# Optimization experiments

Measured on AMD Instinct MI355X. Metric: run time of the kernel, lower is better.

Reference implementation:

```python
import jax, jax.numpy as jnp
import numpy as np

NUM_HEADS = 8
N_POINTS = 9
OFFSET_SCALE = 4.0


def bilinear_sample(fmap_flat, xy, H, W):
    """fmap_flat: (BH, H*W, C) row-major spatial; xy: (BH, S, 2) pixel coords (x, y).
    grid_sample(mode='bilinear', padding_mode='zeros', align_corners=True) equivalent.
    Returns (BH, S, C)."""
    x, y = xy[..., 0], xy[..., 1]
    x0 = jnp.floor(x); y0 = jnp.floor(y)
    x1 = x0 + 1.0;    y1 = y0 + 1.0
    wx1 = x - x0; wx0 = 1.0 - wx1
    wy1 = y - y0; wy0 = 1.0 - wy1

    def corner(xi, yi, wgt):
        valid = (xi >= 0) & (xi <= W - 1) & (yi >= 0) & (yi <= H - 1)
        xi_c = jnp.clip(xi, 0, W - 1).astype(jnp.int32)
        yi_c = jnp.clip(yi, 0, H - 1).astype(jnp.int32)
        idx = yi_c * W + xi_c                                   # (BH, S)
        vals = jnp.take_along_axis(fmap_flat, idx[..., None], axis=1)  # (BH, S, C)
        return vals * (wgt * valid.astype(fmap_flat.dtype))[..., None]

    return (corner(x0, y0, wx0 * wy0) + corner(x1, y0, wx1 * wy0)
            + corner(x0, y1, wx0 * wy1) + corner(x1, y1, wx1 * wy1))


def setup_inputs() -> dict:
    key = jax.random.key(0)
    ks = jax.random.split(key, 10)
    B, N, D = 4, 6400, 256
    Hh, P = NUM_HEADS, N_POINTS
    s = 0.02
    return {
        "x":    jax.random.normal(ks[0], (B, N, D), dtype=jnp.float32),
        "Wq":   jax.random.normal(ks[1], (D, D), dtype=jnp.float32) * s,
        "bq":   jnp.zeros((D,), jnp.float32),
        "Woff": jax.random.normal(ks[2], (Hh * P * 2, D), dtype=jnp.float32) * s,
        "boff": jax.random.normal(ks[3], (Hh * P * 2,), dtype=jnp.float32) * s,
        "Wkv":  jax.random.normal(ks[4], (2 * D, D), dtype=jnp.float32) * s,
        "bkv":  jnp.zeros((2 * D,), jnp.float32),
        "Wout": jax.random.normal(ks[5], (D, D), dtype=jnp.float32) * s,
        "bout": jnp.zeros((D,), jnp.float32),
        "h": 40,
        "w": 160,
    }


def reference(x, Wq, bq, Woff, boff, Wkv, bkv, Wout, bout, h, w):
    B, N, D = x.shape
    H, P = NUM_HEADS, N_POINTS
    hd = D // H

    # queries: (B, H, N, hd)
    q = (x @ Wq.T + bq).reshape(B, N, H, hd).transpose(0, 2, 1, 3)

    # per-query per-head offsets in pixels: (B, N, H, P, 2) (dx, dy)
    offsets = jnp.tanh(x @ Woff.T + boff).reshape(B, N, H, P, 2) * OFFSET_SCALE

    # K/V feature maps via 1x1 conv == per-token linear; split heads, flat spatial
    kv = x @ Wkv.T + bkv                     # (B, N, 2D)
    k = kv[..., :D]
    v = kv[..., D:]
    k_flat = k.reshape(B, N, H, hd).transpose(0, 2, 1, 3).reshape(B * H, N, hd)
    v_flat = v.reshape(B, N, H, hd).transpose(0, 2, 1, 3).reshape(B * H, N, hd)

    # base pixel grid (x, y), row-major over (h, w)
    ys, xs = jnp.meshgrid(jnp.arange(h, dtype=x.dtype), jnp.arange(w, dtype=x.dtype), indexing="ij")
    base_xy = jnp.stack([xs, ys], axis=-1).reshape(N, 2)

    # sampling locations: (B, N, H, P, 2) -> (B*H, N*P, 2)
    sample_xy = base_xy[None, :, None, None, :] + offsets
    sample_xy = sample_xy.transpose(0, 2, 1, 3, 4).reshape(B * H, N * P, 2)

    sampled_k = bilinear_sample(k_flat, sample_xy, h, w).reshape(B, H, N, P, hd)
    sampled_v = bilinear_sample(v_flat, sample_xy, h, w).reshape(B, H, N, P, hd)

    logits = jnp.einsum("bhnd,bhnpd->bhnp", q, sampled_k) * (hd ** -0.5)
    attn = jax.nn.softmax(logits, axis=-1)
    out = jnp.einsum("bhnp,bhnpd->bhnd", attn, sampled_v)   # (B, H, N, hd)
    out = out.transpose(0, 2, 1, 3).reshape(B, N, D)
    return out @ Wout.T + bout
```

## Files before the change

### kernel.cpp

```cpp
#include <hip/hip_runtime.h>
#include <math.h>

#define BSZ    4
#define NTOK   6400
#define DMODEL 256
#define NHEAD  8
#define HDIM   32
#define NPTS   9
#define HSP    40
#define WSP    160
#define KDIM   256
#define MTOT   (BSZ*NTOK)

typedef short  short8  __attribute__((ext_vector_type(8)));
typedef float  floatx4 __attribute__((ext_vector_type(4)));
typedef float  f32x2   __attribute__((ext_vector_type(2)));

__device__ __forceinline__ ushort f2bf(float f) {
    uint u = __float_as_uint(f);
    u = (u + 0x7FFFu + ((u >> 16) & 1u)) >> 16;
    return (ushort)u;
}

__device__ __forceinline__ void unpack8v(uint4 u, f32x2* f) {
    f[0].x = __uint_as_float(u.x << 16); f[0].y = __uint_as_float(u.x & 0xFFFF0000u);
    f[1].x = __uint_as_float(u.y << 16); f[1].y = __uint_as_float(u.y & 0xFFFF0000u);
    f[2].x = __uint_as_float(u.z << 16); f[2].y = __uint_as_float(u.z & 0xFFFF0000u);
    f[3].x = __uint_as_float(u.w << 16); f[3].y = __uint_as_float(u.w & 0xFFFF0000u);
}

__device__ __forceinline__ float dot8(uint4 u, const f32x2* q2) {
    f32x2 a; a.x = 0.f; a.y = 0.f;
    f32x2 t;
    t.x = __uint_as_float(u.x << 16); t.y = __uint_as_float(u.x & 0xFFFF0000u);
    a += t * q2[0];
    t.x = __uint_as_float(u.y << 16); t.y = __uint_as_float(u.y & 0xFFFF0000u);
    a += t * q2[1];
    t.x = __uint_as_float(u.z << 16); t.y = __uint_as_float(u.z & 0xFFFF0000u);
    a += t * q2[2];
    t.x = __uint_as_float(u.w << 16); t.y = __uint_as_float(u.w & 0xFFFF0000u);
    a += t * q2[3];
    return a.x + a.y;
}

#define AS1C(p) ((const __attribute__((address_space(1))) void*)(p))
#define AS3(p)  ((__attribute__((address_space(3))) void*)(p))

__global__ __launch_bounds__(256) void cast_all(
    const float* __restrict__ x,   const float* __restrict__ Wq,
    const float* __restrict__ Woff,const float* __restrict__ Wkv,
    const float* __restrict__ Wout,
    ushort* __restrict__ xb, ushort* __restrict__ wf, ushort* __restrict__ woutb)
{
    const int bid = blockIdx.x;
    const int o = (bid < 1600) ? ((bid >> 3) + (bid & 7) * 200) : bid;
    if (o >= 1625 && o < 1632) {
        const int i = (o - 1625) * 4096 + threadIdx.x * 4;
        ushort4 z; z.x = 0; z.y = 0; z.z = 0; z.w = 0;
        #pragma unroll
        for (int k = 0; k < 4; ++k)
            *(ushort4*)(wf + 400 * 256 + i + k * 1024) = z;
        return;
    }
    const float* src; ushort* dst; int base;
    if      (o < 1600) { src = x;    dst = xb;              base = o; }
    else if (o < 1616) { src = Wq;   dst = wf;              base = o - 1600; }
    else if (o < 1625) { src = Woff; dst = wf + 256 * 256;  base = o - 1616; }
    else if (o < 1664) { src = Wkv;  dst = wf + 512 * 256;  base = o - 1632; }
    else               { src = Wout; dst = woutb;           base = o - 1664; }
    const int i0 = base * 4096 + threadIdx.x * 4;
    float4 v[4];
    #pragma unroll
    for (int k = 0; k < 4; ++k) v[k] = *(const float4*)(src + i0 + k * 1024);
    #pragma unroll
    for (int k = 0; k < 4; ++k) {
        ushort4 o4;
        o4.x = f2bf(v[k].x); o4.y = f2bf(v[k].y);
        o4.z = f2bf(v[k].z); o4.w = f2bf(v[k].w);
        *(ushort4*)(dst + i0 + k * 1024) = o4;
    }
}

template <int MODE>
__global__ __launch_bounds__(256) void gemm64(
    const ushort* __restrict__ Xb,
    const ushort* __restrict__ Wf,
    const float* __restrict__ bq, const float* __restrict__ boff,
    const float* __restrict__ bkv,
    ushort* __restrict__ qb, float* __restrict__ off,
    ushort* __restrict__ kfb, ushort* __restrict__ vfb,
    float* __restrict__ Yout)
{
    constexpr int NBN = (MODE == 0) ? 16 : 4;
    __shared__ ushort As[2][64 * 64];
    __shared__ ushort Bs[2][64 * 64];

    const int tid = threadIdx.x;
    const int bid = blockIdx.x;
    const int xcd = bid & 7;
    const int j   = bid >> 3;
    const int block_n = (j % NBN) * 64;
    const int block_m = (xcd * 50 + j / NBN) * 64;

    const int wave = tid >> 6, lane = tid & 63;
    const int wr = (wave >> 1) * 32, wc = (wave & 1) * 32;
    const int l15 = lane & 15, quad = lane >> 4;

    const int srow  = lane >> 3;
    const int sslot = (lane & 7) ^ srow;

    floatx4 acc[2][2];
    #pragma unroll
    for (int i = 0; i < 2; ++i)
        #pragma unroll
        for (int jj = 0; jj < 2; ++jj) {
            acc[i][jj][0] = 0.f; acc[i][jj][1] = 0.f;
            acc[i][jj][2] = 0.f; acc[i][jj][3] = 0.f;
        }

    auto stage = [&](int buf, int kt) {
        #pragma unroll
        for (int i = 0; i < 2; ++i) {
            const int rb = wave * 16 + i * 8;
            const ushort* sa = Xb + (size_t)(block_m + rb + srow) * KDIM + kt + sslot * 8;
            const ushort* sb = Wf + (size_t)(block_n + rb + srow) * KDIM + kt + sslot * 8;
            __builtin_amdgcn_global_load_lds(AS1C(sa), AS3(&As[buf][rb * 64]), 16, 0, 0);
            __builtin_amdgcn_global_load_lds(AS1C(sb), AS3(&Bs[buf][rb * 64]), 16, 0, 0);
        }
    };

    auto compute = [&](int buf) {
        #pragma unroll
        for (int ks2 = 0; ks2 < 2; ++ks2) {
            short8 af[2], bfr[2];
            #pragma unroll
            for (int f = 0; f < 2; ++f) {
                const int ra  = wr + f * 16 + l15;
                const int rbb = wc + f * 16 + l15;
                const int sl  = (((ks2 * 4 + quad) ^ (l15 & 7))) * 8;
                af[f]  = *(const short8*)&As[buf][ra * 64 + sl];
                bfr[f] = *(const short8*)&Bs[buf][rbb * 64 + sl];
            }
            #pragma unroll
            for (int fm = 0; fm < 2; ++fm)
                #pragma unroll
                for (int fn = 0; fn < 2; ++fn)
                    acc[fm][fn] = __builtin_amdgcn_mfma_f32_16x16x32_bf16(
                        af[fm], bfr[fn], acc[fm][fn], 0, 0, 0);
        }
    };

    stage(0, 0);
    __syncthreads();
    #pragma unroll
    for (int t = 0; t < 3; ++t) {
        stage((t + 1) & 1, (t + 1) * 64);
        compute(t & 1);
        __syncthreads();
    }
    compute(1);

    const int bb  = block_m / NTOK;
    const int nn0 = block_m - bb * NTOK;
    #pragma unroll
    for (int fn = 0; fn < 2; ++fn) {
        const int col = block_n + wc + fn * 16 + l15;
        float bcol;
        if (MODE == 1) {
            bcol = bq[col];
        } else {
            if      (col < 256) bcol = bq[col];
            else if (col < 400) bcol = boff[col - 256];
            else if (col < 512) bcol = 0.f;
            else                bcol = bkv[col - 512];
        }
        #pragma unroll
        for (int fm = 0; fm < 2; ++fm) {
            #pragma unroll
            for (int r = 0; r < 4; ++r) {
                const int rloc = wr + fm * 16 + quad * 4 + r;
                const int row  = block_m + rloc;
                const float val = acc[fm][fn][r] + bcol;
                if (MODE == 1) {
                    Yout[(size_t)row * DMODEL + col] = val;
                } else {
                    if (col < 256) {
                        qb[(size_t)row * DMODEL + col] = f2bf(val);
                    } else if (col < 400) {
                        off[(size_t)row * 144 + (col - 256)] = tanhf(val) * 4.0f;
                    } else if (col >= 512) {
                        const int c2 = col - 512;
                        const int hh = (c2 & 255) >> 5, cc = c2 & 31;
                        const int nn = nn0 + rloc;
                        const size_t o = (((size_t)(bb * NHEAD + hh)) * NTOK + nn) * HDIM + cc;
                        if (c2 < 256) kfb[o] = f2bf(val);
                        else          vfb[o] = f2bf(val);
                    }
                }
            }
        }
    }
}

__global__ __launch_bounds__(256, 3) void deform_attn(
    const ushort* __restrict__ qb,
    const float* __restrict__ off,
    const ushort* __restrict__ kfb,
    const ushort* __restrict__ vfb,
    ushort* __restrict__ attnb)
{
    const int lane = threadIdx.x & 63;
    const int o = ((int)blockIdx.x >> 3) + ((int)blockIdx.x & 7) * 400;
    const int token = o * 8 + (threadIdx.x >> 6) * 2 + (lane >> 5);
    const int h = (lane >> 2) & 7, lc = lane & 3;
    const int b = token / NTOK, n = token % NTOK;

    const uint4 qu = *(const uint4*)(qb + (size_t)token * DMODEL + h * HDIM + lc * 8);
    f32x2 q2[4]; unpack8v(qu, q2);

    const float* ob = off + (size_t)token * 144 + h * (NPTS * 2);
    const float bx = (float)(n % WSP), by = (float)(n / WSP);
    const ushort* kbase = kfb + (size_t)(b * NHEAD + h) * NTOK * HDIM + lc * 8;
    const ushort* vbase = vfb + (size_t)(b * NHEAD + h) * NTOK * HDIM + lc * 8;

    float s = 0.f;
    f32x2 o2[4];
    #pragma unroll
    for (int i = 0; i < 4; ++i) { o2[i].x = 0.f; o2[i].y = 0.f; }

    #pragma unroll
    for (int g = 0; g < 3; ++g) {
        int   idx[3][4];
        float wt[3][4];
        #pragma unroll
        for (int jj = 0; jj < 3; ++jj) {
            const int p = g * 3 + jj;
            const float2 of = *(const float2*)(ob + 2 * p);
            const float sx = bx + of.x, sy = by + of.y;
            const float fx0 = floorf(sx), fy0 = floorf(sy);
            const float wx1 = sx - fx0, wx0 = 1.0f - wx1;
            const float wy1 = sy - fy0, wy0 = 1.0f - wy1;
            const int ix0 = (int)fx0, iy0 = (int)fy0;
            const int ix1 = ix0 + 1, iy1 = iy0 + 1;
            const bool vx0 = (ix0 >= 0) & (ix0 <= WSP - 1);
            const bool vx1 = (ix1 >= 0) & (ix1 <= WSP - 1);
            const bool vy0 = (iy0 >= 0) & (iy0 <= HSP - 1);
            const bool vy1 = (iy1 >= 0) & (iy1 <= HSP - 1);
            const int cx0 = min(max(ix0, 0), WSP - 1);
            const int cx1 = min(max(ix1, 0), WSP - 1);
            const int cy0 = min(max(iy0, 0), HSP - 1);
            const int cy1 = min(max(iy1, 0), HSP - 1);
            wt[jj][0] = wx0 * wy0 * (float)(vx0 && vy0);
            wt[jj][1] = wx1 * wy0 * (float)(vx1 && vy0);
            wt[jj][2] = wx0 * wy1 * (float)(vx0 && vy1);
            wt[jj][3] = wx1 * wy1 * (float)(vx1 && vy1);
            idx[jj][0] = (cy0 * WSP + cx0) * HDIM;
            idx[jj][1] = (cy0 * WSP + cx1) * HDIM;
            idx[jj][2] = (cy1 * WSP + cx0) * HDIM;
            idx[jj][3] = (cy1 * WSP + cx1) * HDIM;
        }

        uint4 ku[12], vu[12];
        #pragma unroll
        for (int jj = 0; jj < 3; ++jj)
            #pragma unroll
            for (int c = 0; c < 4; ++c)
                ku[jj * 4 + c] = *(const uint4*)(kbase + idx[jj][c]);
        #pragma unroll
        for (int jj = 0; jj < 3; ++jj)
            #pragma unroll
            for (int c = 0; c < 4; ++c)
                vu[jj * 4 + c] = *(const uint4*)(vbase + idx[jj][c]);

        float l[3];
        #pragma unroll
        for (int jj = 0; jj < 3; ++jj) {
            float part = wt[jj][0] * dot8(ku[jj * 4 + 0], q2)
                       + wt[jj][1] * dot8(ku[jj * 4 + 1], q2)
                       + wt[jj][2] * dot8(ku[jj * 4 + 2], q2)
                       + wt[jj][3] * dot8(ku[jj * 4 + 3], q2);
            part += __shfl_xor(part, 1, 64);
            part += __shfl_xor(part, 2, 64);
            l[jj] = part * 0.17677669529663687f;
        }

        const float e0 = __expf(l[0]);
        const float e1 = __expf(l[1]);
        const float e2 = __expf(l[2]);
        s += e0 + e1 + e2;
        const float e[3] = {e0, e1, e2};

        #pragma unroll
        for (int jj = 0; jj < 3; ++jj) {
            #pragma unroll
            for (int c = 0; c < 4; ++c) {
                f32x2 vv[4]; unpack8v(vu[jj * 4 + c], vv);
                const float ew = e[jj] * wt[jj][c];
                #pragma unroll
                for (int i = 0; i < 4; ++i) o2[i] += vv[i] * ew;
            }
        }
    }

    const float inv = 1.0f / s;
    uint4 ru;
    ru.x = (uint)f2bf(o2[0].x * inv) | ((uint)f2bf(o2[0].y * inv) << 16);
    ru.y = (uint)f2bf(o2[1].x * inv) | ((uint)f2bf(o2[1].y * inv) << 16);
    ru.z = (uint)f2bf(o2[2].x * inv) | ((uint)f2bf(o2[2].y * inv) << 16);
    ru.w = (uint)f2bf(o2[3].x * inv) | ((uint)f2bf(o2[3].y * inv) << 16);
    *(uint4*)(attnb + (size_t)token * DMODEL + h * HDIM + lc * 8) = ru;
}

extern "C" void kernel_launch(void* const* d_in, const int* in_sizes, int n_in,
                              void* d_out, int out_size, void* d_ws, size_t ws_size,
                              hipStream_t stream) {
    const float* x    = (const float*)d_in[0];
    const float* Wq   = (const float*)d_in[1];
    const float* bq   = (const float*)d_in[2];
    const float* Woff = (const float*)d_in[3];
    const float* boff = (const float*)d_in[4];
    const float* Wkv  = (const float*)d_in[5];
    const float* bkv  = (const float*)d_in[6];
    const float* Wout = (const float*)d_in[7];
    const float* bout = (const float*)d_in[8];

    ushort* xb    = (ushort*)d_ws;
    ushort* qb    = xb + (size_t)MTOT * DMODEL;
    float*  off   = (float*)(qb + (size_t)MTOT * DMODEL);
    ushort* kfb   = (ushort*)(off + (size_t)MTOT * 144);
    ushort* vfb   = kfb + (size_t)MTOT * DMODEL;
    ushort* wf    = vfb + (size_t)MTOT * DMODEL;
    ushort* woutb = wf + 262144;
    ushort* attnb = xb;

    cast_all<<<dim3(1680), dim3(256), 0, stream>>>(x, Wq, Woff, Wkv, Wout,
                                                   xb, wf, woutb);

    gemm64<0><<<dim3(6400), dim3(256), 0, stream>>>(xb, wf, bq, boff, bkv,
                                                    qb, off, kfb, vfb, nullptr);

    deform_attn<<<dim3(3200), dim3(256), 0, stream>>>(qb, off, kfb, vfb, attnb);

    gemm64<1><<<dim3(1600), dim3(256), 0, stream>>>(attnb, woutb, bout,
                                                    nullptr, nullptr, nullptr,
                                                    nullptr, nullptr, nullptr,
                                                    (float*)d_out);
}
```

Baseline: 190.4 us.

## Fuse fp32-to-bf16 cast of x into QKV GEMM and restructure deform_attn loads

Removes the separate pass that converts x to bf16. The first GEMM now loads fp32 rows of x into registers, converts them to bf16 and writes them into swizzled LDS, which saves a full write and re-read of the bf16 copy of x. The weight-only cast kernel shrinks to 80 blocks. deform_attn is reorganised to compute all sampling indices up front and fold the softmax scale into q. It then issues all K gathers before any V gathers and drops the occupancy hint. This adds register pressure, and the A-tile staging becomes synchronous register loads instead of global_load_lds.

```diff
diff --git a/kernel.cpp b/kernel.cpp
--- a/kernel.cpp
+++ b/kernel.cpp
@@ -47,15 +47,13 @@
 #define AS3(p)  ((__attribute__((address_space(3))) void*)(p))
 
 __global__ __launch_bounds__(256) void cast_all(
-    const float* __restrict__ x,   const float* __restrict__ Wq,
-    const float* __restrict__ Woff,const float* __restrict__ Wkv,
-    const float* __restrict__ Wout,
-    ushort* __restrict__ xb, ushort* __restrict__ wf, ushort* __restrict__ woutb)
+    const float* __restrict__ Wq, const float* __restrict__ Woff,
+    const float* __restrict__ Wkv, const float* __restrict__ Wout,
+    ushort* __restrict__ wf, ushort* __restrict__ woutb)
 {
-    const int bid = blockIdx.x;
-    const int o = (bid < 1600) ? ((bid >> 3) + (bid & 7) * 200) : bid;
-    if (o >= 1625 && o < 1632) {
-        const int i = (o - 1625) * 4096 + threadIdx.x * 4;
+    const int o = blockIdx.x;
+    if (o >= 25 && o < 32) {
+        const int i = (o - 25) * 4096 + threadIdx.x * 4;
         ushort4 z; z.x = 0; z.y = 0; z.z = 0; z.w = 0;
         #pragma unroll
         for (int k = 0; k < 4; ++k)
@@ -63,11 +61,10 @@
         return;
     }
     const float* src; ushort* dst; int base;
-    if      (o < 1600) { src = x;    dst = xb;              base = o; }
-    else if (o < 1616) { src = Wq;   dst = wf;              base = o - 1600; }
-    else if (o < 1625) { src = Woff; dst = wf + 256 * 256;  base = o - 1616; }
-    else if (o < 1664) { src = Wkv;  dst = wf + 512 * 256;  base = o - 1632; }
-    else               { src = Wout; dst = woutb;           base = o - 1664; }
+    if      (o < 16) { src = Wq;   dst = wf;              base = o; }
+    else if (o < 25) { src = Woff; dst = wf + 256 * 256;  base = o - 16; }
+    else if (o < 64) { src = Wkv;  dst = wf + 512 * 256;  base = o - 32; }
+    else             { src = Wout; dst = woutb;           base = o - 64; }
     const int i0 = base * 4096 + threadIdx.x * 4;
     float4 v[4];
     #pragma unroll
@@ -83,6 +80,7 @@
 
 template <int MODE>
 __global__ __launch_bounds__(256) void gemm64(
+    const float*  __restrict__ Xf,
     const ushort* __restrict__ Xb,
     const ushort* __restrict__ Wf,
     const float* __restrict__ bq, const float* __restrict__ boff,
@@ -109,6 +107,10 @@
     const int srow  = lane >> 3;
     const int sslot = (lane & 7) ^ srow;
 
+    const int arow = tid >> 2;
+    const int ac16 = (tid & 3) * 16;
+    float4 areg[4];
+
     floatx4 acc[2][2];
     #pragma unroll
     for (int i = 0; i < 2; ++i)
@@ -118,14 +120,41 @@
             acc[i][jj][2] = 0.f; acc[i][jj][3] = 0.f;
         }
 
-    auto stage = [&](int buf, int kt) {
+    auto loadA = [&](int kt) {
+        if (MODE == 0) {
+            const float* s = Xf + (size_t)(block_m + arow) * KDIM + kt + ac16;
+            areg[0] = *(const float4*)(s + 0);
+            areg[1] = *(const float4*)(s + 4);
+            areg[2] = *(const float4*)(s + 8);
+            areg[3] = *(const float4*)(s + 12);
+        }
+    };
+    auto writeA = [&](int buf) {
+        if (MODE == 0) {
+            uint pk[8];
+            #pragma unroll
+            for (int i = 0; i < 4; ++i) {
+                pk[2 * i]     = (uint)f2bf(areg[i].x) | ((uint)f2bf(areg[i].y) << 16);
+                pk[2 * i + 1] = (uint)f2bf(areg[i].z) | ((uint)f2bf(areg[i].w) << 16);
+            }
+            const int r7 = arow & 7;
+            const int s0 = ac16 >> 3;
+            uint4 w0; w0.x = pk[0]; w0.y = pk[1]; w0.z = pk[2]; w0.w = pk[3];
+            uint4 w1; w1.x = pk[4]; w1.y = pk[5]; w1.z = pk[6]; w1.w = pk[7];
+            *(uint4*)&As[buf][arow * 64 + ((s0 ^ r7) * 8)]       = w0;
+            *(uint4*)&As[buf][arow * 64 + (((s0 + 1) ^ r7) * 8)] = w1;
+        }
+    };
+    auto stageB = [&](int buf, int kt) {
         #pragma unroll
         for (int i = 0; i < 2; ++i) {
             const int rb = wave * 16 + i * 8;
-            const ushort* sa = Xb + (size_t)(block_m + rb + srow) * KDIM + kt + sslot * 8;
             const ushort* sb = Wf + (size_t)(block_n + rb + srow) * KDIM + kt + sslot * 8;
-            __builtin_amdgcn_global_load_lds(AS1C(sa), AS3(&As[buf][rb * 64]), 16, 0, 0);
             __builtin_amdgcn_global_load_lds(AS1C(sb), AS3(&Bs[buf][rb * 64]), 16, 0, 0);
+            if (MODE == 1) {
+                const ushort* sa = Xb + (size_t)(block_m + rb + srow) * KDIM + kt + sslot * 8;
+                __builtin_amdgcn_global_load_lds(AS1C(sa), AS3(&As[buf][rb * 64]), 16, 0, 0);
+            }
         }
     };
 
@@ -150,12 +179,16 @@
         }
     };
 
-    stage(0, 0);
+    loadA(0);
+    stageB(0, 0);
+    writeA(0);
     __syncthreads();
     #pragma unroll
     for (int t = 0; t < 3; ++t) {
-        stage((t + 1) & 1, (t + 1) * 64);
+        loadA((t + 1) * 64);
+        stageB((t + 1) & 1, (t + 1) * 64);
         compute(t & 1);
+        writeA((t + 1) & 1);
         __syncthreads();
     }
     compute(1);
@@ -202,7 +235,7 @@
     }
 }
 
-__global__ __launch_bounds__(256, 3) void deform_attn(
+__global__ __launch_bounds__(256) void deform_attn(
     const ushort* __restrict__ qb,
     const float* __restrict__ off,
     const ushort* __restrict__ kfb,
@@ -217,88 +250,73 @@
 
     const uint4 qu = *(const uint4*)(qb + (size_t)token * DMODEL + h * HDIM + lc * 8);
     f32x2 q2[4]; unpack8v(qu, q2);
+    #pragma unroll
+    for (int i = 0; i < 4; ++i) q2[i] *= 0.17677669529663687f;
 
     const float* ob = off + (size_t)token * 144 + h * (NPTS * 2);
     const float bx = (float)(n % WSP), by = (float)(n / WSP);
     const ushort* kbase = kfb + (size_t)(b * NHEAD + h) * NTOK * HDIM + lc * 8;
     const ushort* vbase = vfb + (size_t)(b * NHEAD + h) * NTOK * HDIM + lc * 8;
 
-    float s = 0.f;
+    int   idx[NPTS][4];
+    float wt[NPTS][4];
+    #pragma unroll
+    for (int p = 0; p < NPTS; ++p) {
+        const float2 of = *(const float2*)(ob + 2 * p);
+        const float sx = bx + of.x, sy = by + of.y;
+        const float fx0 = floorf(sx), fy0 = floorf(sy);
+        const float wx1 = sx - fx0, wx0 = 1.0f - wx1;
+        const float wy1 = sy - fy0, wy0 = 1.0f - wy1;
+        const int ix0 = (int)fx0, iy0 = (int)fy0;
+        const int ix1 = ix0 + 1, iy1 = iy0 + 1;
+        const bool vx0 = (ix0 >= 0) & (ix0 <= WSP - 1);
+        const bool vx1 = (ix1 >= 0) & (ix1 <= WSP - 1);
+        const bool vy0 = (iy0 >= 0) & (iy0 <= HSP - 1);
+        const bool vy1 = (iy1 >= 0) & (iy1 <= HSP - 1);
+        const int cx0 = min(max(ix0, 0), WSP - 1);
+        const int cx1 = min(max(ix1, 0), WSP - 1);
+        const int cy0 = min(max(iy0, 0), HSP - 1);
+        const int cy1 = min(max(iy1, 0), HSP - 1);
+        wt[p][0] = wx0 * wy0 * (float)(vx0 && vy0);
+        wt[p][1] = wx1 * wy0 * (float)(vx1 && vy0);
+        wt[p][2] = wx0 * wy1 * (float)(vx0 && vy1);
+        wt[p][3] = wx1 * wy1 * (float)(vx1 && vy1);
+        idx[p][0] = (cy0 * WSP + cx0) * HDIM;
+        idx[p][1] = (cy0 * WSP + cx1) * HDIM;
+        idx[p][2] = (cy1 * WSP + cx0) * HDIM;
+        idx[p][3] = (cy1 * WSP + cx1) * HDIM;
+    }
+
+    float l[NPTS];
+    #pragma unroll
+    for (int p = 0; p < NPTS; ++p) {
+        const uint4 k0 = *(const uint4*)(kbase + idx[p][0]);
+        const uint4 k1 = *(const uint4*)(kbase + idx[p][1]);
+        const uint4 k2 = *(const uint4*)(kbase + idx[p][2]);
+        const uint4 k3 = *(const uint4*)(kbase + idx[p][3]);
+        float part = wt[p][0] * dot8(k0, q2) + wt[p][1] * dot8(k1, q2)
+                   + wt[p][2] * dot8(k2, q2) + wt[p][3] * dot8(k3, q2);
+        part += __shfl_xor(part, 1, 64);
+        part += __shfl_xor(part, 2, 64);
+        l[p] = part;
+    }
+
+    float s = 0.f, e[NPTS];
+    #pragma unroll
+    for (int p = 0; p < NPTS; ++p) { e[p] = __expf(l[p]); s += e[p]; }
+
     f32x2 o2[4];
     #pragma unroll
     for (int i = 0; i < 4; ++i) { o2[i].x = 0.f; o2[i].y = 0.f; }
-
-    #pragma unroll
-    for (int g = 0; g < 3; ++g) {
-        int   idx[3][4];
-        float wt[3][4];
-        #pragma unroll
-        for (int jj = 0; jj < 3; ++jj) {
-            const int p = g * 3 + jj;
-            const float2 of = *(const float2*)(ob + 2 * p);
-            const float sx = bx + of.x, sy = by + of.y;
-            const float fx0 = floorf(sx), fy0 = floorf(sy);
-            const float wx1 = sx - fx0, wx0 = 1.0f - wx1;
-            const float wy1 = sy - fy0, wy0 = 1.0f - wy1;
-            const int ix0 = (int)fx0, iy0 = (int)fy0;
-            const int ix1 = ix0 + 1, iy1 = iy0 + 1;
-            const bool vx0 = (ix0 >= 0) & (ix0 <= WSP - 1);
-            const bool vx1 = (ix1 >= 0) & (ix1 <= WSP - 1);
-            const bool vy0 = (iy0 >= 0) & (iy0 <= HSP - 1);
-            const bool vy1 = (iy1 >= 0) & (iy1 <= HSP - 1);
-            const int cx0 = min(max(ix0, 0), WSP - 1);
-            const int cx1 = min(max(ix1, 0), WSP - 1);
-            const int cy0 = min(max(iy0, 0), HSP - 1);
-            const int cy1 = min(max(iy1, 0), HSP - 1);
-            wt[jj][0] = wx0 * wy0 * (float)(vx0 && vy0);
-            wt[jj][1] = wx1 * wy0 * (float)(vx1 && vy0);
-            wt[jj][2] = wx0 * wy1 * (float)(vx0 && vy1);
-            wt[jj][3] = wx1 * wy1 * (float)(vx1 && vy1);
-            idx[jj][0] = (cy0 * WSP + cx0) * HDIM;
-            idx[jj][1] = (cy0 * WSP + cx1) * HDIM;
-            idx[jj][2] = (cy1 * WSP + cx0) * HDIM;
-            idx[jj][3] = (cy1 * WSP + cx1) * HDIM;
-        }
-
-        uint4 ku[12], vu[12];
-        #pragma unroll
-        for (int jj = 0; jj < 3; ++jj)
-            #pragma unroll
-            for (int c = 0; c < 4; ++c)
-                ku[jj * 4 + c] = *(const uint4*)(kbase + idx[jj][c]);
-        #pragma unroll
-        for (int jj = 0; jj < 3; ++jj)
-            #pragma unroll
-            for (int c = 0; c < 4; ++c)
-                vu[jj * 4 + c] = *(const uint4*)(vbase + idx[jj][c]);
-
-        float l[3];
-        #pragma unroll
-        for (int jj = 0; jj < 3; ++jj) {
-            float part = wt[jj][0] * dot8(ku[jj * 4 + 0], q2)
-                       + wt[jj][1] * dot8(ku[jj * 4 + 1], q2)
-                       + wt[jj][2] * dot8(ku[jj * 4 + 2], q2)
-                       + wt[jj][3] * dot8(ku[jj * 4 + 3], q2);
-            part += __shfl_xor(part, 1, 64);
-            part += __shfl_xor(part, 2, 64);
-            l[jj] = part * 0.17677669529663687f;
-        }
-
-        const float e0 = __expf(l[0]);
-        const float e1 = __expf(l[1]);
-        const float e2 = __expf(l[2]);
-        s += e0 + e1 + e2;
-        const float e[3] = {e0, e1, e2};
-
-        #pragma unroll
-        for (int jj = 0; jj < 3; ++jj) {
-            #pragma unroll
-            for (int c = 0; c < 4; ++c) {
-                f32x2 vv[4]; unpack8v(vu[jj * 4 + c], vv);
-                const float ew = e[jj] * wt[jj][c];
-                #pragma unroll
-                for (int i = 0; i < 4; ++i) o2[i] += vv[i] * ew;
-            }
+    #pragma unroll
+    for (int p = 0; p < NPTS; ++p) {
+        #pragma unroll
+        for (int c = 0; c < 4; ++c) {
+            const uint4 vu = *(const uint4*)(vbase + idx[p][c]);
+            f32x2 vv[4]; unpack8v(vu, vv);
+            const float ew = e[p] * wt[p][c];
+            #pragma unroll
+            for (int i = 0; i < 4; ++i) o2[i] += vv[i] * ew;
         }
     }
 
@@ -324,24 +342,22 @@
     const float* Wout = (const float*)d_in[7];
     const float* bout = (const float*)d_in[8];
 
-    ushort* xb    = (ushort*)d_ws;
-    ushort* qb    = xb + (size_t)MTOT * DMODEL;
+    ushort* attnb = (ushort*)d_ws;
+    ushort* qb    = attnb + (size_t)MTOT * DMODEL;
     float*  off   = (float*)(qb + (size_t)MTOT * DMODEL);
     ushort* kfb   = (ushort*)(off + (size_t)MTOT * 144);
     ushort* vfb   = kfb + (size_t)MTOT * DMODEL;
     ushort* wf    = vfb + (size_t)MTOT * DMODEL;
     ushort* woutb = wf + 262144;
-    ushort* attnb = xb;
-
-    cast_all<<<dim3(1680), dim3(256), 0, stream>>>(x, Wq, Woff, Wkv, Wout,
-                                                   xb, wf, woutb);
-
-    gemm64<0><<<dim3(6400), dim3(256), 0, stream>>>(xb, wf, bq, boff, bkv,
+
+    cast_all<<<dim3(80), dim3(256), 0, stream>>>(Wq, Woff, Wkv, Wout, wf, woutb);
+
+    gemm64<0><<<dim3(6400), dim3(256), 0, stream>>>(x, nullptr, wf, bq, boff, bkv,
                                                     qb, off, kfb, vfb, nullptr);
 
     deform_attn<<<dim3(3200), dim3(256), 0, stream>>>(qb, off, kfb, vfb, attnb);
 
-    gemm64<1><<<dim3(1600), dim3(256), 0, stream>>>(attnb, woutb, bout,
+    gemm64<1><<<dim3(1600), dim3(256), 0, stream>>>(nullptr, attnb, woutb, bout,
                                                     nullptr, nullptr, nullptr,
                                                     nullptr, nullptr, nullptr,
                                                     (float*)d_out);
```

New measurement: 202.0 us. 6.1% more time.

## Fuse output projection into deformable attention and pack offsets as int16

Applied to the files above, without the earlier changes.

The output projection GEMM is folded into the attention kernel. Each block computes 16 tokens of attention into a swizzled LDS tile, then runs bf16 MFMA against Wout and writes the final fp32 output, so the attn intermediate round trip and one launch go away. Offsets are stored as int16 fixed point (tanh scaled by 16384) instead of fp32, which halves offset traffic at some precision cost. The attention loop now handles all 9 points per token with K and V loads interleaved with compute. The launch-bounds occupancy hint is dropped, and each block rereads Wout from global/L2.

```diff
diff --git a/kernel.cpp b/kernel.cpp
--- a/kernel.cpp
+++ b/kernel.cpp
@@ -81,17 +81,15 @@
     }
 }
 
-template <int MODE>
-__global__ __launch_bounds__(256) void gemm64(
+__global__ __launch_bounds__(256) void gemm_qokv(
     const ushort* __restrict__ Xb,
     const ushort* __restrict__ Wf,
     const float* __restrict__ bq, const float* __restrict__ boff,
     const float* __restrict__ bkv,
-    ushort* __restrict__ qb, float* __restrict__ off,
-    ushort* __restrict__ kfb, ushort* __restrict__ vfb,
-    float* __restrict__ Yout)
+    ushort* __restrict__ qb, short* __restrict__ offp,
+    ushort* __restrict__ kfb, ushort* __restrict__ vfb)
 {
-    constexpr int NBN = (MODE == 0) ? 16 : 4;
+    constexpr int NBN = 16;
     __shared__ ushort As[2][64 * 64];
     __shared__ ushort Bs[2][64 * 64];
 
@@ -166,14 +164,10 @@
     for (int fn = 0; fn < 2; ++fn) {
         const int col = block_n + wc + fn * 16 + l15;
         float bcol;
-        if (MODE == 1) {
-            bcol = bq[col];
-        } else {
-            if      (col < 256) bcol = bq[col];
-            else if (col < 400) bcol = boff[col - 256];
-            else if (col < 512) bcol = 0.f;
-            else                bcol = bkv[col - 512];
-        }
+        if      (col < 256) bcol = bq[col];
+        else if (col < 400) bcol = boff[col - 256];
+        else if (col < 512) bcol = 0.f;
+        else                bcol = bkv[col - 512];
         #pragma unroll
         for (int fm = 0; fm < 2; ++fm) {
             #pragma unroll
@@ -181,62 +175,66 @@
                 const int rloc = wr + fm * 16 + quad * 4 + r;
                 const int row  = block_m + rloc;
                 const float val = acc[fm][fn][r] + bcol;
-                if (MODE == 1) {
-                    Yout[(size_t)row * DMODEL + col] = val;
-                } else {
-                    if (col < 256) {
-                        qb[(size_t)row * DMODEL + col] = f2bf(val);
-                    } else if (col < 400) {
-                        off[(size_t)row * 144 + (col - 256)] = tanhf(val) * 4.0f;
-                    } else if (col >= 512) {
-                        const int c2 = col - 512;
-                        const int hh = (c2 & 255) >> 5, cc = c2 & 31;
-                        const int nn = nn0 + rloc;
-                        const size_t o = (((size_t)(bb * NHEAD + hh)) * NTOK + nn) * HDIM + cc;
-                        if (c2 < 256) kfb[o] = f2bf(val);
-                        else          vfb[o] = f2bf(val);
-                    }
+                if (col < 256) {
+                    qb[(size_t)row * DMODEL + col] = f2bf(val);
+                } else if (col < 400) {
+                    offp[(size_t)row * 144 + (col - 256)] =
+                        (short)__float2int_rn(tanhf(val) * 16384.0f);
+                } else if (col >= 512) {
+                    const int c2 = col - 512;
+                    const int hh = (c2 & 255) >> 5, cc = c2 & 31;
+                    const int nn = nn0 + rloc;
+                    const size_t o = (((size_t)(bb * NHEAD + hh)) * NTOK + nn) * HDIM + cc;
+                    if (c2 < 256) kfb[o] = f2bf(val);
+                    else          vfb[o] = f2bf(val);
                 }
             }
         }
     }
 }
 
-__global__ __launch_bounds__(256, 3) void deform_attn(
+__global__ __launch_bounds__(256) void deform_attn_out(
     const ushort* __restrict__ qb,
-    const float* __restrict__ off,
+    const short* __restrict__ offp,
     const ushort* __restrict__ kfb,
     const ushort* __restrict__ vfb,
-    ushort* __restrict__ attnb)
+    const ushort* __restrict__ woutb,
+    const float* __restrict__ bout,
+    float* __restrict__ out)
 {
-    const int lane = threadIdx.x & 63;
-    const int o = ((int)blockIdx.x >> 3) + ((int)blockIdx.x & 7) * 400;
-    const int token = o * 8 + (threadIdx.x >> 6) * 2 + (lane >> 5);
-    const int h = (lane >> 2) & 7, lc = lane & 3;
-    const int b = token / NTOK, n = token % NTOK;
-
-    const uint4 qu = *(const uint4*)(qb + (size_t)token * DMODEL + h * HDIM + lc * 8);
-    f32x2 q2[4]; unpack8v(qu, q2);
-
-    const float* ob = off + (size_t)token * 144 + h * (NPTS * 2);
-    const float bx = (float)(n % WSP), by = (float)(n / WSP);
-    const ushort* kbase = kfb + (size_t)(b * NHEAD + h) * NTOK * HDIM + lc * 8;
-    const ushort* vbase = vfb + (size_t)(b * NHEAD + h) * NTOK * HDIM + lc * 8;
-
-    float s = 0.f;
-    f32x2 o2[4];
-    #pragma unroll
-    for (int i = 0; i < 4; ++i) { o2[i].x = 0.f; o2[i].y = 0.f; }
-
-    #pragma unroll
-    for (int g = 0; g < 3; ++g) {
-        int   idx[3][4];
-        float wt[3][4];
-        #pragma unroll
-        for (int jj = 0; jj < 3; ++jj) {
-            const int p = g * 3 + jj;
-            const float2 of = *(const float2*)(ob + 2 * p);
-            const float sx = bx + of.x, sy = by + of.y;
+    __shared__ ushort A16[16 * 256];
+
+    const int tid  = threadIdx.x;
+    const int wave = tid >> 6, lane = tid & 63;
+    const int o    = ((int)blockIdx.x >> 3) + ((int)blockIdx.x & 7) * 200;
+    const int tok0 = o * 16;
+
+    const int h  = (lane >> 2) & 7, lc = lane & 3;
+
+    #pragma unroll
+    for (int it = 0; it < 2; ++it) {
+        const int tloc  = it * 8 + wave * 2 + (lane >> 5);
+        const int token = tok0 + tloc;
+        const int b = token / NTOK, n = token % NTOK;
+
+        const uint4 qu = *(const uint4*)(qb + (size_t)token * DMODEL + h * HDIM + lc * 8);
+        f32x2 q2[4]; unpack8v(qu, q2);
+        #pragma unroll
+        for (int i = 0; i < 4; ++i) q2[i] *= 0.17677669529663687f;
+
+        const short* ob = offp + (size_t)token * 144 + h * (NPTS * 2);
+        const float bx = (float)(n % WSP), by = (float)(n / WSP);
+        const ushort* kbase = kfb + (size_t)(b * NHEAD + h) * NTOK * HDIM + lc * 8;
+        const ushort* vbase = vfb + (size_t)(b * NHEAD + h) * NTOK * HDIM + lc * 8;
+
+        int   idx[NPTS][4];
+        float wt[NPTS][4];
+        #pragma unroll
+        for (int p = 0; p < NPTS; ++p) {
+            const int u = *(const int*)(ob + 2 * p);
+            const float ofx = (float)((short)(u & 0xFFFF)) * (1.0f / 4096.0f);
+            const float ofy = (float)(u >> 16) * (1.0f / 4096.0f);
+            const float sx = bx + ofx, sy = by + ofy;
             const float fx0 = floorf(sx), fy0 = floorf(sy);
             const float wx1 = sx - fx0, wx0 = 1.0f - wx1;
             const float wy1 = sy - fy0, wy0 = 1.0f - wy1;
@@ -250,65 +248,97 @@
             const int cx1 = min(max(ix1, 0), WSP - 1);
             const int cy0 = min(max(iy0, 0), HSP - 1);
             const int cy1 = min(max(iy1, 0), HSP - 1);
-            wt[jj][0] = wx0 * wy0 * (float)(vx0 && vy0);
-            wt[jj][1] = wx1 * wy0 * (float)(vx1 && vy0);
-            wt[jj][2] = wx0 * wy1 * (float)(vx0 && vy1);
-            wt[jj][3] = wx1 * wy1 * (float)(vx1 && vy1);
-            idx[jj][0] = (cy0 * WSP + cx0) * HDIM;
-            idx[jj][1] = (cy0 * WSP + cx1) * HDIM;
-            idx[jj][2] = (cy1 * WSP + cx0) * HDIM;
-            idx[jj][3] = (cy1 * WSP + cx1) * HDIM;
-        }
-
-        uint4 ku[12], vu[12];
-        #pragma unroll
-        for (int jj = 0; jj < 3; ++jj)
-            #pragma unroll
-            for (int c = 0; c < 4; ++c)
-                ku[jj * 4 + c] = *(const uint4*)(kbase + idx[jj][c]);
-        #pragma unroll
-        for (int jj = 0; jj < 3; ++jj)
-            #pragma unroll
-            for (int c = 0; c < 4; ++c)
-                vu[jj * 4 + c] = *(const uint4*)(vbase + idx[jj][c]);
-
-        float l[3];
-        #pragma unroll
-        for (int jj = 0; jj < 3; ++jj) {
-            float part = wt[jj][0] * dot8(ku[jj * 4 + 0], q2)
-                       + wt[jj][1] * dot8(ku[jj * 4 + 1], q2)
-                       + wt[jj][2] * dot8(ku[jj * 4 + 2], q2)
-                       + wt[jj][3] * dot8(ku[jj * 4 + 3], q2);
+            wt[p][0] = wx0 * wy0 * (float)(vx0 && vy0);
+            wt[p][1] = wx1 * wy0 * (float)(vx1 && vy0);
+            wt[p][2] = wx0 * wy1 * (float)(vx0 && vy1);
+            wt[p][3] = wx1 * wy1 * (float)(vx1 && vy1);
+            idx[p][0] = (cy0 * WSP + cx0) * HDIM;
+            idx[p][1] = (cy0 * WSP + cx1) * HDIM;
+            idx[p][2] = (cy1 * WSP + cx0) * HDIM;
+            idx[p][3] = (cy1 * WSP + cx1) * HDIM;
+        }
+
+        float l[NPTS];
+        #pragma unroll
+        for (int p = 0; p < NPTS; ++p) {
+            const uint4 k0 = *(const uint4*)(kbase + idx[p][0]);
+            const uint4 k1 = *(const uint4*)(kbase + idx[p][1]);
+            const uint4 k2 = *(const uint4*)(kbase + idx[p][2]);
+            const uint4 k3 = *(const uint4*)(kbase + idx[p][3]);
+            float part = wt[p][0] * dot8(k0, q2) + wt[p][1] * dot8(k1, q2)
+                       + wt[p][2] * dot8(k2, q2) + wt[p][3] * dot8(k3, q2);
             part += __shfl_xor(part, 1, 64);
             part += __shfl_xor(part, 2, 64);
-            l[jj] = part * 0.17677669529663687f;
-        }
-
-        const float e0 = __expf(l[0]);
-        const float e1 = __expf(l[1]);
-        const float e2 = __expf(l[2]);
-        s += e0 + e1 + e2;
-        const float e[3] = {e0, e1, e2};
-
-        #pragma unroll
-        for (int jj = 0; jj < 3; ++jj) {
+            l[p] = part;
+        }
+
+        float s = 0.f, e[NPTS];
+        #pragma unroll
+        for (int p = 0; p < NPTS; ++p) { e[p] = __expf(l[p]); s += e[p]; }
+
+        f32x2 o2[4];
+        #pragma unroll
+        for (int i = 0; i < 4; ++i) { o2[i].x = 0.f; o2[i].y = 0.f; }
+        #pragma unroll
+        for (int p = 0; p < NPTS; ++p) {
             #pragma unroll
             for (int c = 0; c < 4; ++c) {
-                f32x2 vv[4]; unpack8v(vu[jj * 4 + c], vv);
-                const float ew = e[jj] * wt[jj][c];
+                const uint4 vu = *(const uint4*)(vbase + idx[p][c]);
+                f32x2 vv[4]; unpack8v(vu, vv);
+                const float ew = e[p] * wt[p][c];
                 #pragma unroll
                 for (int i = 0; i < 4; ++i) o2[i] += vv[i] * ew;
             }
         }
-    }
-
-    const float inv = 1.0f / s;
-    uint4 ru;
-    ru.x = (uint)f2bf(o2[0].x * inv) | ((uint)f2bf(o2[0].y * inv) << 16);
-    ru.y = (uint)f2bf(o2[1].x * inv) | ((uint)f2bf(o2[1].y * inv) << 16);
-    ru.z = (uint)f2bf(o2[2].x * inv) | ((uint)f2bf(o2[2].y * inv) << 16);
-    ru.w = (uint)f2bf(o2[3].x * inv) | ((uint)f2bf(o2[3].y * inv) << 16);
-    *(uint4*)(attnb + (size_t)token * DMODEL + h * HDIM + lc * 8) = ru;
+
+        const float inv = 1.0f / s;
+        uint4 ru;
+        ru.x = (uint)f2bf(o2[0].x * inv) | ((uint)f2bf(o2[0].y * inv) << 16);
+        ru.y = (uint)f2bf(o2[1].x * inv) | ((uint)f2bf(o2[1].y * inv) << 16);
+        ru.z = (uint)f2bf(o2[2].x * inv) | ((uint)f2bf(o2[2].y * inv) << 16);
+        ru.w = (uint)f2bf(o2[3].x * inv) | ((uint)f2bf(o2[3].y * inv) << 16);
+        const int slot = (h * 4 + lc) ^ (tloc & 7);
+        *(uint4*)&A16[tloc * 256 + slot * 8] = ru;
+    }
+
+    __syncthreads();
+
+    const int l15 = lane & 15, quad = lane >> 4;
+
+    short8 af[8];
+    #pragma unroll
+    for (int ks = 0; ks < 8; ++ks) {
+        const int sl = ((ks * 4 + quad) ^ (l15 & 7)) * 8;
+        af[ks] = *(const short8*)&A16[l15 * 256 + sl];
+    }
+
+    floatx4 oacc[4];
+    #pragma unroll
+    for (int fn = 0; fn < 4; ++fn) {
+        oacc[fn][0] = 0.f; oacc[fn][1] = 0.f; oacc[fn][2] = 0.f; oacc[fn][3] = 0.f;
+    }
+    #pragma unroll
+    for (int fn = 0; fn < 4; ++fn) {
+        const int col = wave * 64 + fn * 16 + l15;
+        #pragma unroll
+        for (int ks = 0; ks < 8; ++ks) {
+            const short8 bfr = *(const short8*)(woutb + (size_t)col * 256
+                                                + ks * 32 + quad * 8);
+            oacc[fn] = __builtin_amdgcn_mfma_f32_16x16x32_bf16(
+                af[ks], bfr, oacc[fn], 0, 0, 0);
+        }
+    }
+
+    #pragma unroll
+    for (int fn = 0; fn < 4; ++fn) {
+        const int col = wave * 64 + fn * 16 + l15;
+        const float bc = bout[col];
+        #pragma unroll
+        for (int r = 0; r < 4; ++r) {
+            const int t = quad * 4 + r;
+            out[(size_t)(tok0 + t) * DMODEL + col] = oacc[fn][r] + bc;
+        }
+    }
 }
 
 extern "C" void kernel_launch(void* const* d_in, const int* in_sizes, int n_in,
@@ -326,23 +356,19 @@
 
     ushort* xb    = (ushort*)d_ws;
     ushort* qb    = xb + (size_t)MTOT * DMODEL;
-    float*  off   = (float*)(qb + (size_t)MTOT * DMODEL);
-    ushort* kfb   = (ushort*)(off + (size_t)MTOT * 144);
+    short*  offp  = (short*)(qb + (size_t)MTOT * DMODEL);
+    ushort* kfb   = (ushort*)(offp + (size_t)MTOT * 144);
     ushort* vfb   = kfb + (size_t)MTOT * DMODEL;
     ushort* wf    = vfb + (size_t)MTOT * DMODEL;
     ushort* woutb = wf + 262144;
-    ushort* attnb = xb;
 
     cast_all<<<dim3(1680), dim3(256), 0, stream>>>(x, Wq, Woff, Wkv, Wout,
                                                    xb, wf, woutb);
 
-    gemm64<0><<<dim3(6400), dim3(256), 0, stream>>>(xb, wf, bq, boff, bkv,
-                                                    qb, off, kfb, vfb, nullptr);
-
-    deform_attn<<<dim3(3200), dim3(256), 0, stream>>>(qb, off, kfb, vfb, attnb);
-
-    gemm64<1><<<dim3(1600), dim3(256), 0, stream>>>(attnb, woutb, bout,
-                                                    nullptr, nullptr, nullptr,
-                                                    nullptr, nullptr, nullptr,
-                                                    (float*)d_out);
-}
+    gemm_qokv<<<dim3(6400), dim3(256), 0, stream>>>(xb, wf, bq, boff, bkv,
+                                                    qb, offp, kfb, vfb);
+
+    deform_attn_out<<<dim3(1600), dim3(256), 0, stream>>>(qb, offp, kfb, vfb,
+                                                          woutb, bout,
+                                                          (float*)d_out);
+}
```

New measurement: 207.2 us. 1.09x slower.
